# Kernel optimization log

Hardware: AMD Instinct MI355X
Metric: run time of the kernel (lower is better)

## Reference

```python
import jax, jax.numpy as jnp
import numpy as np

E = 1024      # embed_dim
H = 16        # num_heads
DH = E // H   # head_dim = 64
B, T = 2, 2048


def setup_inputs() -> dict:
    key = jax.random.key(0)
    ks = jax.random.split(key, 9)
    s = 0.02
    return {
        "hidden_states": jax.random.normal(ks[0], (B, T, E), dtype=jnp.float32),
        "Wq": jax.random.normal(ks[1], (E, E), dtype=jnp.float32) * s,
        "bq": jax.random.normal(ks[2], (E,), dtype=jnp.float32) * s,
        "Wk": jax.random.normal(ks[3], (E, E), dtype=jnp.float32) * s,
        "bk": jax.random.normal(ks[4], (E,), dtype=jnp.float32) * s,
        "Wv": jax.random.normal(ks[5], (E, E), dtype=jnp.float32) * s,
        "bv": jax.random.normal(ks[6], (E,), dtype=jnp.float32) * s,
        "Wo": jax.random.normal(ks[7], (E, E), dtype=jnp.float32) * s,
        "bo": jax.random.normal(ks[8], (E,), dtype=jnp.float32) * s,
    }


def reference(hidden_states, Wq, bq, Wk, bk, Wv, bv, Wo, bo):
    # Faithful to the source, including its bugs:
    #  - q scaled by head_dim**-0.5 AND scores divided by sqrt(head_dim) -> net 1/head_dim
    #  - softmax output assigned to a dead variable; raw scores used for AV matmul
    b, t, _ = hidden_states.shape
    scaling = DH ** -0.5
    q = (hidden_states @ Wq.T + bq) * scaling            # [b, t, E]
    k = hidden_states @ Wk.T + bk
    v = hidden_states @ Wv.T + bv

    def split_heads(x):  # [b, t, E] -> [b, H, t, DH]
        return x.reshape(b, t, H, DH).transpose(0, 2, 1, 3)

    qh, kh, vh = split_heads(q), split_heads(k), split_heads(v)
    attn = jnp.einsum("bhtd,bhsd->bhts", qh, kh) / jnp.sqrt(jnp.float32(DH))
    # (softmax computed in source but its result is discarded)
    out = jnp.einsum("bhts,bhsd->bhtd", attn, vh)        # [b, H, t, DH]
    out = out.transpose(0, 2, 1, 3).reshape(b, t, E)
    return out @ Wo.T + bo
```

## Files before the change

### kernel.cpp

```cpp
#include <hip/hip_runtime.h>

#define E_  1024
#define H_  16
#define B_  2
#define T_  2048
#define BT_ (B_*T_)

typedef __bf16 bf16x8 __attribute__((ext_vector_type(8)));
typedef float  f32x4  __attribute__((ext_vector_type(4)));
typedef unsigned short u16x8 __attribute__((ext_vector_type(8)));

static __device__ __forceinline__ unsigned short f2bf(float x){
  unsigned int u = __float_as_uint(x);
  u += 0x7fffu + ((u >> 16) & 1u);
  return (unsigned short)(u >> 16);
}
static __device__ __forceinline__ float bf2f(unsigned short s){
  return __uint_as_float(((unsigned int)s) << 16);
}

static __device__ __forceinline__ void gld16(const unsigned short* g, unsigned short* l){
  __builtin_amdgcn_global_load_lds(
      (const __attribute__((address_space(1))) void*)g,
      (__attribute__((address_space(3))) void*)l, 16, 0, 0);
}

__global__ __launch_bounds__(256)
void cast_hidden(const float* __restrict__ in, unsigned short* __restrict__ out){
  int i = (blockIdx.x * 256 + threadIdx.x) * 8;
  float4 v0 = *(const float4*)(in + i);
  float4 v1 = *(const float4*)(in + i + 4);
  u16x8 o;
  o[0]=f2bf(v0.x); o[1]=f2bf(v0.y); o[2]=f2bf(v0.z); o[3]=f2bf(v0.w);
  o[4]=f2bf(v1.x); o[5]=f2bf(v1.y); o[6]=f2bf(v1.z); o[7]=f2bf(v1.w);
  *(u16x8*)(out + i) = o;
}

__global__ __launch_bounds__(256)
void cast_weights(const float* __restrict__ Wq, const float* __restrict__ Wk,
                  const float* __restrict__ Wv, const float* __restrict__ Wo,
                  unsigned short* __restrict__ wqkv, unsigned short* __restrict__ wob){
  int bid = blockIdx.x;
  int w = bid >> 9;
  int off = (bid & 511) * 2048 + threadIdx.x * 8;
  const float* src = (w==0) ? Wq : (w==1) ? Wk : (w==2) ? Wv : Wo;
  unsigned short* dst = (w==3) ? wob : (wqkv + (size_t)w * 1048576);
  float4 v0 = *(const float4*)(src + off);
  float4 v1 = *(const float4*)(src + off + 4);
  u16x8 o;
  o[0]=f2bf(v0.x); o[1]=f2bf(v0.y); o[2]=f2bf(v0.z); o[3]=f2bf(v0.w);
  o[4]=f2bf(v1.x); o[5]=f2bf(v1.y); o[6]=f2bf(v1.z); o[7]=f2bf(v1.w);
  *(u16x8*)(dst + off) = o;
}

__global__ __launch_bounds__(256)
void gemm_qkv(const unsigned short* __restrict__ A,
              const unsigned short* __restrict__ Wqkv,
              const float* __restrict__ bq, const float* __restrict__ bk,
              const float* __restrict__ bv,
              unsigned short* __restrict__ Q, unsigned short* __restrict__ Ko,
              unsigned short* __restrict__ Vo)
{
  __shared__ unsigned short As[4096];
  __shared__ unsigned short Bs[4096];
  const int tid = threadIdx.x;
  const int wv = tid >> 6, ln = tid & 63;
  const int wr = wv >> 1, wc = wv & 1;
  const int lr = ln & 15;
  const int lk8 = (ln >> 4) * 8;
  const int bm = blockIdx.x, bn = blockIdx.y;
  const size_t arow0 = (size_t)bm * 128;
  const size_t brow0 = (size_t)bn * 128;
  const int K = 1024;

  f32x4 acc[4][4];
  #pragma unroll
  for (int m = 0; m < 4; ++m)
    #pragma unroll
    for (int n = 0; n < 4; ++n) acc[m][n] = (f32x4){0.f,0.f,0.f,0.f};

  for (int k0 = 0; k0 < K; k0 += 32) {
    #pragma unroll
    for (int i = 0; i < 2; ++i) {
      int c = i*256 + wv*64 + ln;
      int row = c >> 2, off = (c & 3) * 8;
      gld16(A    + (arow0 + row) * K + k0 + off, As + (size_t)(i*256 + wv*64) * 8);
      gld16(Wqkv + (brow0 + row) * K + k0 + off, Bs + (size_t)(i*256 + wv*64) * 8);
    }
    __syncthreads();
    bf16x8 af[4], bf[4];
    #pragma unroll
    for (int m = 0; m < 4; ++m) af[m] = *(const bf16x8*)&As[(wr*64 + m*16 + lr)*32 + lk8];
    #pragma unroll
    for (int n = 0; n < 4; ++n) bf[n] = *(const bf16x8*)&Bs[(wc*64 + n*16 + lr)*32 + lk8];
    #pragma unroll
    for (int m = 0; m < 4; ++m)
      #pragma unroll
      for (int n = 0; n < 4; ++n)
        acc[m][n] = __builtin_amdgcn_mfma_f32_16x16x32_bf16(af[m], bf[n], acc[m][n], 0, 0, 0);
    __syncthreads();
  }

  const int which = bn >> 3;
  const float* bias = (which==0) ? bq : (which==1) ? bk : bv;
  unsigned short* Out = (which==0) ? Q : (which==1) ? Ko : Vo;
  const float scale = (which==0) ? 0.125f : 1.0f;
  #pragma unroll
  for (int n = 0; n < 4; ++n) {
    int col = (bn & 7)*128 + wc*64 + n*16 + lr;
    float bvv = bias[col];
    #pragma unroll
    for (int m = 0; m < 4; ++m) {
      int row0 = bm*128 + wr*64 + m*16 + (ln >> 4) * 4;
      #pragma unroll
      for (int r = 0; r < 4; ++r)
        Out[(size_t)(row0 + r) * 1024 + col] = f2bf((acc[m][n][r] + bvv) * scale);
    }
  }
}

__global__ __launch_bounds__(256)
void gemm_o(const unsigned short* __restrict__ A,
            const unsigned short* __restrict__ Bw,
            const float* __restrict__ bias, float* __restrict__ C)
{
  __shared__ unsigned short As[2048];
  __shared__ unsigned short Bs[4096];
  const int tid = threadIdx.x;
  const int wv = tid >> 6, ln = tid & 63;
  const int wr = wv >> 1, wc = wv & 1;
  const int lr = ln & 15;
  const int lk8 = (ln >> 4) * 8;
  const int bm = blockIdx.x, bn = blockIdx.y;
  const size_t arow0 = (size_t)bm * 64;
  const size_t brow0 = (size_t)bn * 128;
  const int K = 1024;

  f32x4 acc[2][4];
  #pragma unroll
  for (int m = 0; m < 2; ++m)
    #pragma unroll
    for (int n = 0; n < 4; ++n) acc[m][n] = (f32x4){0.f,0.f,0.f,0.f};

  for (int k0 = 0; k0 < K; k0 += 32) {
    {
      int row = tid >> 2, off = (tid & 3) * 8;
      gld16(A + (arow0 + row) * K + k0 + off, As + (size_t)(wv*64) * 8);
    }
    #pragma unroll
    for (int i = 0; i < 2; ++i) {
      int c = i*256 + wv*64 + ln;
      int row = c >> 2, off = (c & 3) * 8;
      gld16(Bw + (brow0 + row) * K + k0 + off, Bs + (size_t)(i*256 + wv*64) * 8);
    }
    __syncthreads();
    bf16x8 af[2], bf[4];
    #pragma unroll
    for (int m = 0; m < 2; ++m) af[m] = *(const bf16x8*)&As[(wr*32 + m*16 + lr)*32 + lk8];
    #pragma unroll
    for (int n = 0; n < 4; ++n) bf[n] = *(const bf16x8*)&Bs[(wc*64 + n*16 + lr)*32 + lk8];
    #pragma unroll
    for (int m = 0; m < 2; ++m)
      #pragma unroll
      for (int n = 0; n < 4; ++n)
        acc[m][n] = __builtin_amdgcn_mfma_f32_16x16x32_bf16(af[m], bf[n], acc[m][n], 0, 0, 0);
    __syncthreads();
  }

  #pragma unroll
  for (int n = 0; n < 4; ++n) {
    int col = bn*128 + wc*64 + n*16 + lr;
    float bvv = bias[col];
    #pragma unroll
    for (int m = 0; m < 2; ++m) {
      int row0 = bm*64 + wr*32 + m*16 + (ln >> 4) * 4;
      #pragma unroll
      for (int r = 0; r < 4; ++r)
        C[(size_t)(row0 + r) * 1024 + col] = acc[m][n][r] + bvv;
    }
  }
}

__global__ __launch_bounds__(256)
void ktv_partial(const unsigned short* __restrict__ Kmat,
                 const unsigned short* __restrict__ Vmat,
                 float* __restrict__ Mpart)
{
  __shared__ float Ks[32][64];
  __shared__ float Vs[32][64];
  const int tid   = threadIdx.x;
  const int bh    = blockIdx.x;
  const int chunk = blockIdx.y;
  const int b = bh >> 4, h = bh & 15;
  const int d2  = tid & 63;
  const int d1b = (tid >> 6) * 16;
  float acc[16];
  #pragma unroll
  for (int i = 0; i < 16; ++i) acc[i] = 0.f;
  const int row = tid >> 3, off = (tid & 7) * 8;
  const size_t base = ((size_t)b * T_) * E_ + (size_t)h * 64;

  for (int t0 = chunk * 256; t0 < chunk * 256 + 256; t0 += 32) {
    u16x8 kv = *(const u16x8*)(Kmat + base + (size_t)(t0 + row) * E_ + off);
    u16x8 vv = *(const u16x8*)(Vmat + base + (size_t)(t0 + row) * E_ + off);
    #pragma unroll
    for (int j = 0; j < 8; ++j) { Ks[row][off+j] = bf2f(kv[j]); Vs[row][off+j] = bf2f(vv[j]); }
    __syncthreads();
    for (int tt = 0; tt < 32; ++tt) {
      float vvv = Vs[tt][d2];
      #pragma unroll
      for (int i = 0; i < 16; ++i) acc[i] += Ks[tt][d1b + i] * vvv;
    }
    __syncthreads();
  }
  float* mp = Mpart + ((size_t)bh * 8 + chunk) * 4096;
  #pragma unroll
  for (int i = 0; i < 16; ++i) mp[(d1b + i) * 64 + d2] = acc[i];
}

__global__ __launch_bounds__(256)
void ktv_reduce(const float* __restrict__ Mpart, float* __restrict__ Mfin){
  const int bh = blockIdx.x;
  for (int i = threadIdx.x; i < 4096; i += 256) {
    float s = 0.f;
    #pragma unroll
    for (int c = 0; c < 8; ++c) s += Mpart[((size_t)bh * 8 + c) * 4096 + i];
    Mfin[(size_t)bh * 4096 + i] = s * 0.125f;
  }
}

__global__ __launch_bounds__(256)
void qm_kernel(const unsigned short* __restrict__ Q,
               const float* __restrict__ Mfin,
               unsigned short* __restrict__ O)
{
  __shared__ float Ms[64][64];
  __shared__ float Qs[32][64];
  const int tid = threadIdx.x;
  const int rb  = blockIdx.x;
  const int h   = blockIdx.y;
  const int b   = rb >> 6;
  const int t0  = (rb & 63) * 32;
  const float* mf = Mfin + ((size_t)(b * 16 + h)) * 4096;
  for (int i = tid; i < 4096; i += 256) Ms[i >> 6][i & 63] = mf[i];
  const int row = tid >> 3, off = (tid & 7) * 8;
  const size_t base = ((size_t)b * T_) * E_ + (size_t)h * 64;
  u16x8 qv = *(const u16x8*)(Q + base + (size_t)(t0 + row) * E_ + off);
  #pragma unroll
  for (int j = 0; j < 8; ++j) Qs[row][off + j] = bf2f(qv[j]);
  __syncthreads();
  const int d2 = tid & 63;
  const int r0 = (tid >> 6) * 8;
  for (int rr = r0; rr < r0 + 8; ++rr) {
    float s = 0.f;
    #pragma unroll
    for (int d1 = 0; d1 < 64; ++d1) s += Qs[rr][d1] * Ms[d1][d2];
    O[base + (size_t)(t0 + rr) * E_ + d2] = f2bf(s);
  }
}

extern "C" void kernel_launch(void* const* d_in, const int* in_sizes, int n_in,
                              void* d_out, int out_size, void* d_ws, size_t ws_size,
                              hipStream_t stream)
{
  const float* hidden = (const float*)d_in[0];
  const float* Wq = (const float*)d_in[1];
  const float* bq = (const float*)d_in[2];
  const float* Wk = (const float*)d_in[3];
  const float* bk = (const float*)d_in[4];
  const float* Wv = (const float*)d_in[5];
  const float* bv = (const float*)d_in[6];
  const float* Wo = (const float*)d_in[7];
  const float* bo = (const float*)d_in[8];
  float* out = (float*)d_out;

  const size_t SZ_ACT = (size_t)BT_ * E_;
  const size_t SZ_W   = (size_t)E_ * E_;

  char* p = (char*)d_ws;
  unsigned short* hb   = (unsigned short*)p; p += SZ_ACT * 2;
  unsigned short* wqkv = (unsigned short*)p; p += SZ_W * 3 * 2;
  unsigned short* wob  = (unsigned short*)p; p += SZ_W * 2;
  unsigned short* qb   = (unsigned short*)p; p += SZ_ACT * 2;
  unsigned short* kb   = (unsigned short*)p; p += SZ_ACT * 2;
  unsigned short* vb   = (unsigned short*)p; p += SZ_ACT * 2;
  unsigned short* ob   = (unsigned short*)p; p += SZ_ACT * 2;
  float* Mpart = (float*)p; p += (size_t)32 * 8 * 4096 * 4;
  float* Mfin  = (float*)p; p += (size_t)32 * 4096 * 4;

  cast_hidden <<<2048, 256, 0, stream>>>(hidden, hb);
  cast_weights<<<2048, 256, 0, stream>>>(Wq, Wk, Wv, Wo, wqkv, wob);

  gemm_qkv<<<dim3(32, 24), 256, 0, stream>>>(hb, wqkv, bq, bk, bv, qb, kb, vb);

  ktv_partial<<<dim3(32, 8), 256, 0, stream>>>(kb, vb, Mpart);
  ktv_reduce <<<32, 256, 0, stream>>>(Mpart, Mfin);
  qm_kernel  <<<dim3(128, 16), 256, 0, stream>>>(qb, Mfin, ob);

  gemm_o<<<dim3(64, 8), 256, 0, stream>>>(ob, wob, bo, out);
}
```

Baseline: 112.0 us.

## Fold per-head K^T V matrix into output projection weights; merge cast kernels

Instead of computing O = Q·M per head and then multiplying by Wo, the per-batch effective weight W2 = blockdiag(M_h)·Wo^T is precomputed (small per-head 64x64 by 64x1024 products). The final GEMM then reads Q directly against this batch-specific weight, which removes the qm_kernel pass and its intermediate activation write and read. The two cast kernels are also merged into one launch. This adds an extra bf16 rounding of the combined weight and a small extra kernel, and each batch now needs its own weight matrix.

```diff
diff --git a/kernel.cpp b/kernel.cpp
--- a/kernel.cpp
+++ b/kernel.cpp
@@ -26,25 +26,23 @@
 }
 
 __global__ __launch_bounds__(256)
-void cast_hidden(const float* __restrict__ in, unsigned short* __restrict__ out){
-  int i = (blockIdx.x * 256 + threadIdx.x) * 8;
-  float4 v0 = *(const float4*)(in + i);
-  float4 v1 = *(const float4*)(in + i + 4);
-  u16x8 o;
-  o[0]=f2bf(v0.x); o[1]=f2bf(v0.y); o[2]=f2bf(v0.z); o[3]=f2bf(v0.w);
-  o[4]=f2bf(v1.x); o[5]=f2bf(v1.y); o[6]=f2bf(v1.z); o[7]=f2bf(v1.w);
-  *(u16x8*)(out + i) = o;
-}
-
-__global__ __launch_bounds__(256)
-void cast_weights(const float* __restrict__ Wq, const float* __restrict__ Wk,
-                  const float* __restrict__ Wv, const float* __restrict__ Wo,
-                  unsigned short* __restrict__ wqkv, unsigned short* __restrict__ wob){
+void cast_all(const float* __restrict__ hidden,
+              const float* __restrict__ Wq, const float* __restrict__ Wk,
+              const float* __restrict__ Wv, const float* __restrict__ Wo,
+              unsigned short* __restrict__ hb,
+              unsigned short* __restrict__ wqkv, unsigned short* __restrict__ wob){
   int bid = blockIdx.x;
-  int w = bid >> 9;
-  int off = (bid & 511) * 2048 + threadIdx.x * 8;
-  const float* src = (w==0) ? Wq : (w==1) ? Wk : (w==2) ? Wv : Wo;
-  unsigned short* dst = (w==3) ? wob : (wqkv + (size_t)w * 1048576);
+  const float* src;
+  unsigned short* dst;
+  int off;
+  if (bid < 2048) {
+    src = hidden; dst = hb; off = bid * 2048 + threadIdx.x * 8;
+  } else {
+    int w = (bid - 2048) >> 9;
+    off = ((bid - 2048) & 511) * 2048 + threadIdx.x * 8;
+    src = (w==0) ? Wq : (w==1) ? Wk : (w==2) ? Wv : Wo;
+    dst = (w==3) ? wob : (wqkv + (size_t)w * 1048576);
+  }
   float4 v0 = *(const float4*)(src + off);
   float4 v1 = *(const float4*)(src + off + 4);
   u16x8 o;
@@ -120,68 +118,6 @@
 }
 
 __global__ __launch_bounds__(256)
-void gemm_o(const unsigned short* __restrict__ A,
-            const unsigned short* __restrict__ Bw,
-            const float* __restrict__ bias, float* __restrict__ C)
-{
-  __shared__ unsigned short As[2048];
-  __shared__ unsigned short Bs[4096];
-  const int tid = threadIdx.x;
-  const int wv = tid >> 6, ln = tid & 63;
-  const int wr = wv >> 1, wc = wv & 1;
-  const int lr = ln & 15;
-  const int lk8 = (ln >> 4) * 8;
-  const int bm = blockIdx.x, bn = blockIdx.y;
-  const size_t arow0 = (size_t)bm * 64;
-  const size_t brow0 = (size_t)bn * 128;
-  const int K = 1024;
-
-  f32x4 acc[2][4];
-  #pragma unroll
-  for (int m = 0; m < 2; ++m)
-    #pragma unroll
-    for (int n = 0; n < 4; ++n) acc[m][n] = (f32x4){0.f,0.f,0.f,0.f};
-
-  for (int k0 = 0; k0 < K; k0 += 32) {
-    {
-      int row = tid >> 2, off = (tid & 3) * 8;
-      gld16(A + (arow0 + row) * K + k0 + off, As + (size_t)(wv*64) * 8);
-    }
-    #pragma unroll
-    for (int i = 0; i < 2; ++i) {
-      int c = i*256 + wv*64 + ln;
-      int row = c >> 2, off = (c & 3) * 8;
-      gld16(Bw + (brow0 + row) * K + k0 + off, Bs + (size_t)(i*256 + wv*64) * 8);
-    }
-    __syncthreads();
-    bf16x8 af[2], bf[4];
-    #pragma unroll
-    for (int m = 0; m < 2; ++m) af[m] = *(const bf16x8*)&As[(wr*32 + m*16 + lr)*32 + lk8];
-    #pragma unroll
-    for (int n = 0; n < 4; ++n) bf[n] = *(const bf16x8*)&Bs[(wc*64 + n*16 + lr)*32 + lk8];
-    #pragma unroll
-    for (int m = 0; m < 2; ++m)
-      #pragma unroll
-      for (int n = 0; n < 4; ++n)
-        acc[m][n] = __builtin_amdgcn_mfma_f32_16x16x32_bf16(af[m], bf[n], acc[m][n], 0, 0, 0);
-    __syncthreads();
-  }
-
-  #pragma unroll
-  for (int n = 0; n < 4; ++n) {
-    int col = bn*128 + wc*64 + n*16 + lr;
-    float bvv = bias[col];
-    #pragma unroll
-    for (int m = 0; m < 2; ++m) {
-      int row0 = bm*64 + wr*32 + m*16 + (ln >> 4) * 4;
-      #pragma unroll
-      for (int r = 0; r < 4; ++r)
-        C[(size_t)(row0 + r) * 1024 + col] = acc[m][n][r] + bvv;
-    }
-  }
-}
-
-__global__ __launch_bounds__(256)
 void ktv_partial(const unsigned short* __restrict__ Kmat,
                  const unsigned short* __restrict__ Vmat,
                  float* __restrict__ Mpart)
@@ -230,32 +166,105 @@
 }
 
 __global__ __launch_bounds__(256)
-void qm_kernel(const unsigned short* __restrict__ Q,
-               const float* __restrict__ Mfin,
-               unsigned short* __restrict__ O)
-{
-  __shared__ float Ms[64][64];
-  __shared__ float Qs[32][64];
+void w2s_kernel(const float* __restrict__ Mfin, const unsigned short* __restrict__ wob,
+                unsigned short* __restrict__ w2st)
+{
+  __shared__ float MsT[64][64];
+  __shared__ unsigned short Wos[64][64];
   const int tid = threadIdx.x;
-  const int rb  = blockIdx.x;
-  const int h   = blockIdx.y;
-  const int b   = rb >> 6;
-  const int t0  = (rb & 63) * 32;
-  const float* mf = Mfin + ((size_t)(b * 16 + h)) * 4096;
-  for (int i = tid; i < 4096; i += 256) Ms[i >> 6][i & 63] = mf[i];
-  const int row = tid >> 3, off = (tid & 7) * 8;
-  const size_t base = ((size_t)b * T_) * E_ + (size_t)h * 64;
-  u16x8 qv = *(const u16x8*)(Q + base + (size_t)(t0 + row) * E_ + off);
-  #pragma unroll
-  for (int j = 0; j < 8; ++j) Qs[row][off + j] = bf2f(qv[j]);
+  const int bh  = blockIdx.x;
+  const int j0  = blockIdx.y * 64;
+  const int b = bh >> 4, h = bh & 15;
+  const float* mf = Mfin + (size_t)bh * 4096;
+
+  #pragma unroll
+  for (int i0 = 0; i0 < 16; i0 += 4) {
+    float4 v = *(const float4*)(mf + tid*16 + i0);
+    int d1 = tid >> 2;
+    int d2 = (tid & 3) * 16 + i0;
+    MsT[d2+0][d1] = v.x; MsT[d2+1][d1] = v.y; MsT[d2+2][d1] = v.z; MsT[d2+3][d1] = v.w;
+  }
+  {
+    int j = tid >> 2, c0 = (tid & 3) * 16;
+    const unsigned short* src = wob + (size_t)(j0 + j) * 1024 + h*64 + c0;
+    *(u16x8*)&Wos[j][c0]     = *(const u16x8*)(src);
+    *(u16x8*)&Wos[j][c0 + 8] = *(const u16x8*)(src + 8);
+  }
   __syncthreads();
-  const int d2 = tid & 63;
-  const int r0 = (tid >> 6) * 8;
-  for (int rr = r0; rr < r0 + 8; ++rr) {
+
+  const int d1 = tid & 63;
+  const int jbase = (tid >> 6) * 16;
+  unsigned short* outp = w2st + ((size_t)b << 20) + (size_t)h * 64 + d1;
+  #pragma unroll
+  for (int jj = 0; jj < 16; ++jj) {
+    int j = jbase + jj;
     float s = 0.f;
     #pragma unroll
-    for (int d1 = 0; d1 < 64; ++d1) s += Qs[rr][d1] * Ms[d1][d2];
-    O[base + (size_t)(t0 + rr) * E_ + d2] = f2bf(s);
+    for (int d2 = 0; d2 < 64; ++d2) s += MsT[d2][d1] * bf2f(Wos[j][d2]);
+    outp[(size_t)(j0 + j) * 1024] = f2bf(s);
+  }
+}
+
+__global__ __launch_bounds__(256)
+void gemm_final(const unsigned short* __restrict__ Qm,
+                const unsigned short* __restrict__ w2st,
+                const float* __restrict__ bo, float* __restrict__ C)
+{
+  __shared__ unsigned short As[2048];
+  __shared__ unsigned short Bs[4096];
+  const int tid = threadIdx.x;
+  const int wv = tid >> 6, ln = tid & 63;
+  const int wr = wv >> 1, wc = wv & 1;
+  const int lr = ln & 15;
+  const int lk8 = (ln >> 4) * 8;
+  const int bm = blockIdx.x, bn = blockIdx.y;
+  const unsigned short* Bw = w2st + ((size_t)(bm >> 5) << 20);
+  const size_t arow0 = (size_t)bm * 64;
+  const size_t brow0 = (size_t)bn * 128;
+  const int K = 1024;
+
+  f32x4 acc[2][4];
+  #pragma unroll
+  for (int m = 0; m < 2; ++m)
+    #pragma unroll
+    for (int n = 0; n < 4; ++n) acc[m][n] = (f32x4){0.f,0.f,0.f,0.f};
+
+  for (int k0 = 0; k0 < K; k0 += 32) {
+    {
+      int row = tid >> 2, off = (tid & 3) * 8;
+      gld16(Qm + (arow0 + row) * K + k0 + off, As + (size_t)(wv*64) * 8);
+    }
+    #pragma unroll
+    for (int i = 0; i < 2; ++i) {
+      int c = i*256 + wv*64 + ln;
+      int row = c >> 2, off = (c & 3) * 8;
+      gld16(Bw + (brow0 + row) * K + k0 + off, Bs + (size_t)(i*256 + wv*64) * 8);
+    }
+    __syncthreads();
+    bf16x8 af[2], bf[4];
+    #pragma unroll
+    for (int m = 0; m < 2; ++m) af[m] = *(const bf16x8*)&As[(wr*32 + m*16 + lr)*32 + lk8];
+    #pragma unroll
+    for (int n = 0; n < 4; ++n) bf[n] = *(const bf16x8*)&Bs[(wc*64 + n*16 + lr)*32 + lk8];
+    #pragma unroll
+    for (int m = 0; m < 2; ++m)
+      #pragma unroll
+      for (int n = 0; n < 4; ++n)
+        acc[m][n] = __builtin_amdgcn_mfma_f32_16x16x32_bf16(af[m], bf[n], acc[m][n], 0, 0, 0);
+    __syncthreads();
+  }
+
+  #pragma unroll
+  for (int n = 0; n < 4; ++n) {
+    int col = bn*128 + wc*64 + n*16 + lr;
+    float bvv = bo[col];
+    #pragma unroll
+    for (int m = 0; m < 2; ++m) {
+      int row0 = bm*64 + wr*32 + m*16 + (ln >> 4) * 4;
+      #pragma unroll
+      for (int r = 0; r < 4; ++r)
+        C[(size_t)(row0 + r) * 1024 + col] = acc[m][n][r] + bvv;
+    }
   }
 }
 
@@ -284,18 +293,17 @@
   unsigned short* qb   = (unsigned short*)p; p += SZ_ACT * 2;
   unsigned short* kb   = (unsigned short*)p; p += SZ_ACT * 2;
   unsigned short* vb   = (unsigned short*)p; p += SZ_ACT * 2;
-  unsigned short* ob   = (unsigned short*)p; p += SZ_ACT * 2;
+  unsigned short* w2st = (unsigned short*)p; p += SZ_W * 2 * 2;
   float* Mpart = (float*)p; p += (size_t)32 * 8 * 4096 * 4;
   float* Mfin  = (float*)p; p += (size_t)32 * 4096 * 4;
 
-  cast_hidden <<<2048, 256, 0, stream>>>(hidden, hb);
-  cast_weights<<<2048, 256, 0, stream>>>(Wq, Wk, Wv, Wo, wqkv, wob);
+  cast_all<<<4096, 256, 0, stream>>>(hidden, Wq, Wk, Wv, Wo, hb, wqkv, wob);
 
   gemm_qkv<<<dim3(32, 24), 256, 0, stream>>>(hb, wqkv, bq, bk, bv, qb, kb, vb);
 
   ktv_partial<<<dim3(32, 8), 256, 0, stream>>>(kb, vb, Mpart);
   ktv_reduce <<<32, 256, 0, stream>>>(Mpart, Mfin);
-  qm_kernel  <<<dim3(128, 16), 256, 0, stream>>>(qb, Mfin, ob);
-
-  gemm_o<<<dim3(64, 8), 256, 0, stream>>>(ob, wob, bo, out);
-}
+  w2s_kernel <<<dim3(32, 16), 256, 0, stream>>>(Mfin, wob, w2st);
+
+  gemm_final<<<dim3(64, 8), 256, 0, stream>>>(qb, w2st, bo, out);
+}
```

Result: slower. 118.9 us (+6.2%).
